# Kernel tuning notes

Measured on AMD Instinct MI355X. Metric: run time of the kernel, lower is better.

Reference implementation:

```python
import jax, jax.numpy as jnp
import numpy as np

N = 100000
E = 1600000
IN_C, HID, OUT_C = 3, 64, 1


def setup_inputs() -> dict:
    key = jax.random.key(0)
    ks = jax.random.split(key, 12)
    x = jax.random.normal(ks[0], (N, IN_C), dtype=jnp.float32)
    edge_index = jax.random.randint(ks[1], (2, E), 0, N, dtype=jnp.int64)

    def glorot(k, shape):
        lim = np.sqrt(6.0 / (shape[0] + shape[1]))
        return jax.random.uniform(k, shape, jnp.float32, -lim, lim)

    return {
        "x": x,
        "edge_index": edge_index,
        "W1": glorot(ks[2], (IN_C, HID)), "b1": jnp.zeros((HID,), jnp.float32),
        "W2": glorot(ks[3], (HID, HID)), "b2": jnp.zeros((HID,), jnp.float32),
        "W3": glorot(ks[4], (HID, HID)), "b3": jnp.zeros((HID,), jnp.float32),
        "Wm1": glorot(ks[5], (HID, HID)), "bm1": jnp.zeros((HID,), jnp.float32),
        "Wm2": glorot(ks[6], (HID, OUT_C)), "bm2": jnp.zeros((OUT_C,), jnp.float32),
    }


def gcn_conv(x, src, dst, W, b):
    """PyG GCNConv: symmetric normalization with self-loops, linear, scatter-add, bias."""
    n = x.shape[0]
    loop = jnp.arange(n, dtype=src.dtype)
    s = jnp.concatenate([src, loop])
    d = jnp.concatenate([dst, loop])
    h = x @ W  # (N, out)
    deg = jax.ops.segment_sum(jnp.ones(s.shape[0], dtype=h.dtype), d, num_segments=n)
    dinv = jnp.where(deg > 0, 1.0 / jnp.sqrt(jnp.where(deg > 0, deg, 1.0)), 0.0)
    norm = dinv[s] * dinv[d]  # (E+N,)
    out = jax.ops.segment_sum(h[s] * norm[:, None], d, num_segments=n)
    return out + b


def reference(x, edge_index, W1, b1, W2, b2, W3, b3, Wm1, bm1, Wm2, bm2):
    src, dst = edge_index[0], edge_index[1]
    # 3 GCN layers with ReLU (dropout inactive in eval mode)
    h = jax.nn.relu(gcn_conv(x, src, dst, W1, b1))
    h = jax.nn.relu(gcn_conv(h, src, dst, W2, b2))
    h = jax.nn.relu(gcn_conv(h, src, dst, W3, b3))
    # MLP head + sigmoid
    h = jax.nn.relu(h @ Wm1 + bm1)
    out = jax.nn.sigmoid(h @ Wm2 + bm2)  # (N, 1)
    return out
```

## Files before the change

kernel.cpp:

```cpp
#include <hip/hip_runtime.h>
#include <hip/hip_fp16.h>
#include <math.h>

#define N_NODES 100000
#define N_EDGES 1600000
#define EP (N_EDGES + N_NODES)
#define HID 64
#define NCHUNK 250
#define CE (N_EDGES / NCHUNK)
#define NBUCK 782
#define CAP 2816
#define NTILE (N_NODES / 16)
#define NPN 4

typedef _Float16 half8_t __attribute__((ext_vector_type(8)));
typedef _Float16 half4_t __attribute__((ext_vector_type(4)));
typedef float f32x4_t __attribute__((ext_vector_type(4)));
typedef unsigned long long u64;


__device__ __forceinline__ float fp8_to_f32_1(unsigned b) {
    unsigned s = b >> 7, e = (b >> 3) & 15, m = b & 7;
    float mag = (e == 0) ? (float)m * 0.001953125f
                         : __uint_as_float(((e + 120u) << 23) | (m << 20));
    return s ? -mag : mag;
}

__device__ __forceinline__ unsigned f32_to_fp8_1(float f) {
    unsigned sb = (__float_as_uint(f) >> 31) << 7;
    float a = fabsf(f);
    if (a > 448.f) a = 448.f;
    if (a < 0.001953125f * 0.5f) return sb;
    if (a < 0.015625f) {
        int q = (int)(a * 512.f + 0.5f);
        if (q > 7) return sb | (1u << 3);
        return sb | (unsigned)q;
    }
    unsigned bits = __float_as_uint(a) + (1u << 19);
    int e = (int)((bits >> 23) & 255) - 127;
    unsigned m = (bits >> 20) & 7;
    int ee = e + 7;
    if (ee > 15) { ee = 15; m = 6; }
    return sb | ((unsigned)ee << 3) | m;
}

__device__ __forceinline__ void addp8(float4& a, unsigned w, bool pred) {
    if (pred) {
#if __has_builtin(__builtin_amdgcn_cvt_pk_f32_fp8)
        auto lo = __builtin_amdgcn_cvt_pk_f32_fp8((int)w, false);
        auto hi = __builtin_amdgcn_cvt_pk_f32_fp8((int)w, true);
        a.x += lo[0]; a.y += lo[1]; a.z += hi[0]; a.w += hi[1];
#else
        a.x += fp8_to_f32_1(w & 255);
        a.y += fp8_to_f32_1((w >> 8) & 255);
        a.z += fp8_to_f32_1((w >> 16) & 255);
        a.w += fp8_to_f32_1(w >> 24);
#endif
    }
}

__device__ __forceinline__ unsigned pack_fp8x4(float a, float b, float c, float d) {
#if __has_builtin(__builtin_amdgcn_cvt_pk_fp8_f32)
    int v = 0;
    v = __builtin_amdgcn_cvt_pk_fp8_f32(a, b, v, false);
    v = __builtin_amdgcn_cvt_pk_fp8_f32(c, d, v, true);
    return (unsigned)v;
#else
    return f32_to_fp8_1(a) | (f32_to_fp8_1(b) << 8) |
           (f32_to_fp8_1(c) << 16) | (f32_to_fp8_1(d) << 24);
#endif
}


__global__ void init_kernel(int* __restrict__ gcur, int* __restrict__ csr) {
    int t = threadIdx.x;
    for (int b = t; b < NBUCK; b += 512) gcur[b] = b * CAP;
    if (t < 64) csr[EP + t] = 0;
}

__global__ __launch_bounds__(1024)
void scatter_kernel(const int* __restrict__ src, const int* __restrict__ dst,
                    int* __restrict__ gcur, unsigned* __restrict__ ebuf) {
    __shared__ int hist[NBUCK];
    __shared__ int cur[NBUCK];
    const int tid = threadIdx.x, c = blockIdx.x;
    for (int b = tid; b < NBUCK; b += 1024) hist[b] = 0;
    __syncthreads();
    const int4* d4p = (const int4*)(dst + c * CE);
    const int4* s4p = (const int4*)(src + c * CE);
    const int t0 = tid, t1 = tid + 1024;
    const bool v1 = t1 < CE / 4;
    int4 d0 = d4p[t0], s0 = s4p[t0];
    int4 d1, s1;
    if (v1) { d1 = d4p[t1]; s1 = s4p[t1]; }
    atomicAdd(&hist[d0.x >> 7], 1);
    atomicAdd(&hist[d0.y >> 7], 1);
    atomicAdd(&hist[d0.z >> 7], 1);
    atomicAdd(&hist[d0.w >> 7], 1);
    if (v1) {
        atomicAdd(&hist[d1.x >> 7], 1);
        atomicAdd(&hist[d1.y >> 7], 1);
        atomicAdd(&hist[d1.z >> 7], 1);
        atomicAdd(&hist[d1.w >> 7], 1);
    }
    __syncthreads();
    for (int b = tid; b < NBUCK; b += 1024)
        cur[b] = hist[b] ? atomicAdd(&gcur[b], hist[b]) : 0;
    __syncthreads();
    {
        int p0 = atomicAdd(&cur[d0.x >> 7], 1);
        ebuf[p0] = ((unsigned)(d0.x & 127) << 17) | (unsigned)s0.x;
        int p1 = atomicAdd(&cur[d0.y >> 7], 1);
        ebuf[p1] = ((unsigned)(d0.y & 127) << 17) | (unsigned)s0.y;
        int p2 = atomicAdd(&cur[d0.z >> 7], 1);
        ebuf[p2] = ((unsigned)(d0.z & 127) << 17) | (unsigned)s0.z;
        int p3 = atomicAdd(&cur[d0.w >> 7], 1);
        ebuf[p3] = ((unsigned)(d0.w & 127) << 17) | (unsigned)s0.w;
    }
    if (v1) {
        int p0 = atomicAdd(&cur[d1.x >> 7], 1);
        ebuf[p0] = ((unsigned)(d1.x & 127) << 17) | (unsigned)s1.x;
        int p1 = atomicAdd(&cur[d1.y >> 7], 1);
        ebuf[p1] = ((unsigned)(d1.y & 127) << 17) | (unsigned)s1.y;
        int p2 = atomicAdd(&cur[d1.z >> 7], 1);
        ebuf[p2] = ((unsigned)(d1.z & 127) << 17) | (unsigned)s1.z;
        int p3 = atomicAdd(&cur[d1.w >> 7], 1);
        ebuf[p3] = ((unsigned)(d1.w & 127) << 17) | (unsigned)s1.w;
    }
}

__global__ __launch_bounds__(256)
void rankfill_kernel(const unsigned* __restrict__ ebuf, const int* __restrict__ gcur,
                     int* __restrict__ rowptr, int* __restrict__ csr,
                     float* __restrict__ dinv,
                     const float* __restrict__ x, float4* __restrict__ xd) {
    __shared__ unsigned stash[CAP];
    __shared__ int out[CAP + 128];
    __shared__ int cnt[128];
    __shared__ int cnt2[128];
    __shared__ int rpl8[128];
    __shared__ int wsum[2];
    __shared__ int sR0;
    const int tid = threadIdx.x, b = blockIdx.x;
    if (tid < 128) { cnt[tid] = 0; cnt2[tid] = 0; }
    if (tid == 0) sR0 = 0;
    __syncthreads();

    int acc = 0;
    for (int i = tid; i < b; i += 256) acc += gcur[i] - i * CAP + 128;
    if (acc) atomicAdd(&sR0, acc);

    const int E0 = b * CAP;
    const int RL = gcur[b] - E0;
    for (int off = tid; off < RL; off += 256) {
        unsigned v = ebuf[E0 + off];
        stash[off] = v;
        atomicAdd(&cnt[(v >> 17) & 0x7F], 1);
    }
    __syncthreads();
    const int R0 = sR0;

    const int lane = tid & 63, w = tid >> 6;
    int xcnt = (tid < 128) ? cnt[tid] : 0;
    int inc = xcnt;
#pragma unroll
    for (int off = 1; off < 64; off <<= 1) {
        int y = __shfl_up(inc, off, 64);
        if (lane >= off) inc += y;
    }
    if (lane == 63 && w < 2) wsum[w] = inc;
    __syncthreads();
    if (tid < 128) {
        int base = (w == 1) ? wsum[0] : 0;
        int rel = tid + base + inc - xcnt;
        rpl8[tid] = rel;
        const int n = b * 128 + tid;
        if (n < N_NODES) {
            rowptr[n] = R0 + rel;
            float di = rsqrtf((float)(xcnt + 1));
            dinv[n] = di;
            out[rel + xcnt] = n;
            xd[n] = make_float4(x[n * 3 + 0] * di, x[n * 3 + 1] * di, x[n * 3 + 2] * di, 0.f);
        }
    }
    if (b == NBUCK - 1 && tid == 0) rowptr[N_NODES] = EP;
    __syncthreads();

    for (int off = tid; off < RL; off += 256) {
        unsigned v = stash[off];
        int key = (v >> 17) & 0x7F;
        int r = atomicAdd(&cnt2[key], 1);
        out[rpl8[key] + r] = (int)(v & 0x1FFFFu);
    }
    __syncthreads();

    const int nreal = min(128, N_NODES - b * 128);
    const int lim = RL + nreal;
    for (int i = tid; i < lim; i += 256) csr[R0 + i] = out[i];
}


__device__ __forceinline__ void bfly_store_lds(float4 acc, const float4 b4, float di,
                                               int g, int p, int l, _Float16* __restrict__ tl) {
    acc.x += __shfl_xor(acc.x, 16, 64);
    acc.y += __shfl_xor(acc.y, 16, 64);
    acc.z += __shfl_xor(acc.z, 16, 64);
    acc.w += __shfl_xor(acc.w, 16, 64);
    acc.x += __shfl_xor(acc.x, 32, 64);
    acc.y += __shfl_xor(acc.y, 32, 64);
    acc.z += __shfl_xor(acc.z, 32, 64);
    acc.w += __shfl_xor(acc.w, 32, 64);
    if (g == 0) {
        half4_t hv;
        hv[0] = (_Float16)fmaxf(fmaf(di, acc.x, b4.x), 0.f);
        hv[1] = (_Float16)fmaxf(fmaf(di, acc.y, b4.y), 0.f);
        hv[2] = (_Float16)fmaxf(fmaf(di, acc.z, b4.z), 0.f);
        hv[3] = (_Float16)fmaxf(fmaf(di, acc.w, b4.w), 0.f);
        *(half4_t*)(tl + l * 72 + p * 4) = hv;
    }
}

__device__ __forceinline__ void gather_phase(const unsigned* __restrict__ gfq,
                                             const int* __restrict__ rowptr,
                                             const int* __restrict__ csr,
                                             const float* __restrict__ dinv,
                                             const float* __restrict__ bias,
                                             int n0, int lane, int wid,
                                             _Float16* __restrict__ tl) {
    const int g = lane >> 4, p = lane & 15;
    const int nw = n0 + wid * NPN;
    int rp = rowptr[nw + min(lane, NPN)];
    const float4 b4 = ((const float4*)bias)[p];
    int begv[NPN], cntv[NPN], idxv[NPN];
    int end_prev = __shfl(rp, 0, 64);
#pragma unroll
    for (int i = 0; i < NPN; ++i) {
        int end = __shfl(rp, i + 1, 64);
        begv[i] = end_prev;
        cntv[i] = end - end_prev;
        end_prev = end;
        idxv[i] = (lane < cntv[i]) ? csr[begv[i] + lane] : 0;
    }
    unsigned u[NPN][4];
#pragma unroll
    for (int i = 0; i < NPN; ++i)
#pragma unroll
        for (int k = 0; k < 4; ++k)
            u[i][k] = gfq[(size_t)__shfl(idxv[i], g + 4 * k, 64) * 16 + p];
#pragma unroll
    for (int i = 0; i < NPN; ++i) {
        const int c = cntv[i];
        float4 acc = make_float4(0.f, 0.f, 0.f, 0.f);
        addp8(acc, u[i][0], g + 0 < c);
        addp8(acc, u[i][1], g + 4 < c);
        addp8(acc, u[i][2], g + 8 < c);
        addp8(acc, u[i][3], g + 12 < c);
        if (c > 16) {
#pragma unroll
            for (int k = 4; k < 8; ++k) {
                int e = g + 4 * k;
                int s = __shfl(idxv[i], e, 64);
                addp8(acc, gfq[(size_t)s * 16 + p], e < c);
            }
            if (c > 32) {
                for (int e = 32 + g; e < c; e += 4) {
                    int s = (e < 64) ? __shfl(idxv[i], e, 64) : csr[begv[i] + e];
                    addp8(acc, gfq[(size_t)s * 16 + p], true);
                }
            }
        }
        bfly_store_lds(acc, b4, dinv[nw + i], g, p, wid * NPN + i, tl);
    }
}

__device__ __forceinline__ void mfma_fp8_store(const float* __restrict__ W,
                                               const float* __restrict__ dinv, int n0,
                                               int lane, int wid, int tid,
                                               _Float16* __restrict__ tile,
                                               _Float16* __restrict__ tile2,
                                               unsigned* __restrict__ gf_out) {
    const int kg = lane >> 4, n = lane & 15;
    half8_t B0, B1;
#pragma unroll
    for (int j = 0; j < 8; ++j) {
        B0[j] = (_Float16)W[(kg * 8 + j) * HID + wid * 16 + n];
        B1[j] = (_Float16)W[(32 + kg * 8 + j) * HID + wid * 16 + n];
    }
    half8_t A0 = *(const half8_t*)(tile + n * 72 + kg * 8);
    half8_t A1 = *(const half8_t*)(tile + n * 72 + 32 + kg * 8);
    f32x4_t c = {0.f, 0.f, 0.f, 0.f};
    c = __builtin_amdgcn_mfma_f32_16x16x32_f16(A0, B0, c, 0, 0, 0);
    c = __builtin_amdgcn_mfma_f32_16x16x32_f16(A1, B1, c, 0, 0, 0);
    const int q = lane >> 4;
#pragma unroll
    for (int r = 0; r < 4; ++r)
        tile2[(q * 4 + r) * 72 + wid * 16 + n] = (_Float16)(c[r] * dinv[n0 + q * 4 + r]);
    __syncthreads();
    const int row = tid >> 4, seg = tid & 15;
    uint2 v = *(const uint2*)(tile2 + row * 72 + seg * 4);
    __half2 h0 = *(__half2*)&v.x, h1 = *(__half2*)&v.y;
    float2 f0 = __half22float2(h0), f1 = __half22float2(h1);
    gf_out[(size_t)(n0 + row) * 16 + seg] = pack_fp8x4(f0.x, f0.y, f1.x, f1.y);
}


__global__ __launch_bounds__(256, 8)
void fused_layer1_kernel(const float4* __restrict__ xd, const int* __restrict__ rowptr,
                         const int* __restrict__ csr, const float* __restrict__ dinv,
                         const float* __restrict__ b1, const float* __restrict__ W1,
                         const float* __restrict__ W2, unsigned* __restrict__ gf_out) {
    __shared__ __align__(16) _Float16 tile[16 * 72];
    __shared__ __align__(16) _Float16 tile2[16 * 72];
    const int tid = threadIdx.x;
    const int lane = tid & 63, wid = tid >> 6;
    const int n0 = blockIdx.x * 16;

    const int j = lane >> 4, p0 = lane & 15;
    const int l = wid * 4 + j;
    const int node = n0 + l;
    const int beg = rowptr[node], end = rowptr[node + 1];
    float a0 = 0.f, a1 = 0.f, a2 = 0.f;
    for (int e = beg + p0; e < end; e += 16) {
        float4 v = xd[csr[e]];
        a0 += v.x; a1 += v.y; a2 += v.z;
    }
#pragma unroll
    for (int off = 1; off < 16; off <<= 1) {
        a0 += __shfl_xor(a0, off, 64);
        a1 += __shfl_xor(a1, off, 64);
        a2 += __shfl_xor(a2, off, 64);
    }
    const float dd = dinv[node];
    const float4 w0 = ((const float4*)W1)[p0];
    const float4 w1 = ((const float4*)(W1 + HID))[p0];
    const float4 w2 = ((const float4*)(W1 + 2 * HID))[p0];
    const float4 bb = ((const float4*)b1)[p0];
    half4_t hv;
    hv[0] = (_Float16)fmaxf(fmaf(dd, a0 * w0.x + a1 * w1.x + a2 * w2.x, bb.x), 0.f);
    hv[1] = (_Float16)fmaxf(fmaf(dd, a0 * w0.y + a1 * w1.y + a2 * w2.y, bb.y), 0.f);
    hv[2] = (_Float16)fmaxf(fmaf(dd, a0 * w0.z + a1 * w1.z + a2 * w2.z, bb.z), 0.f);
    hv[3] = (_Float16)fmaxf(fmaf(dd, a0 * w0.w + a1 * w1.w + a2 * w2.w, bb.w), 0.f);
    *(half4_t*)(tile + l * 72 + p0 * 4) = hv;
    __syncthreads();

    mfma_fp8_store(W2, dinv, n0, lane, wid, tid, tile, tile2, gf_out);
}

__global__ __launch_bounds__(256, 8)
void fused_layer_kernel(const unsigned* __restrict__ gf_in, const int* __restrict__ rowptr,
                        const int* __restrict__ csr, const float* __restrict__ dinv,
                        const float* __restrict__ bias, const float* __restrict__ W,
                        unsigned* __restrict__ gf_out) {
    __shared__ __align__(16) _Float16 tile[16 * 72];
    __shared__ __align__(16) _Float16 tile2[16 * 72];
    const int tid = threadIdx.x;
    const int lane = tid & 63, wid = tid >> 6;
    const int n0 = blockIdx.x * 16;

    gather_phase(gf_in, rowptr, csr, dinv, bias, n0, lane, wid, tile);
    __syncthreads();

    mfma_fp8_store(W, dinv, n0, lane, wid, tid, tile, tile2, gf_out);
}


__global__ __launch_bounds__(256, 8)
void fused_final_kernel(const unsigned* __restrict__ gf_in, const int* __restrict__ rowptr,
                        const int* __restrict__ csr, const float* __restrict__ dinv,
                        const float* __restrict__ b3, const float* __restrict__ Wm1,
                        const float* __restrict__ bm1, const float* __restrict__ Wm2,
                        const float* __restrict__ bm2, float* __restrict__ out) {
    __shared__ __align__(16) _Float16 tile[16 * 72];
    __shared__ float redbuf[4][16];
    const int tid = threadIdx.x;
    const int lane = tid & 63, wid = tid >> 6;
    const int n0 = blockIdx.x * 16;

    gather_phase(gf_in, rowptr, csr, dinv, b3, n0, lane, wid, tile);
    __syncthreads();

    const int kg = lane >> 4, n = lane & 15;
    half8_t B0, B1;
#pragma unroll
    for (int j = 0; j < 8; ++j) {
        B0[j] = (_Float16)Wm1[(kg * 8 + j) * HID + wid * 16 + n];
        B1[j] = (_Float16)Wm1[(32 + kg * 8 + j) * HID + wid * 16 + n];
    }
    half8_t A0 = *(const half8_t*)(tile + n * 72 + kg * 8);
    half8_t A1 = *(const half8_t*)(tile + n * 72 + 32 + kg * 8);
    f32x4_t c = {0.f, 0.f, 0.f, 0.f};
    c = __builtin_amdgcn_mfma_f32_16x16x32_f16(A0, B0, c, 0, 0, 0);
    c = __builtin_amdgcn_mfma_f32_16x16x32_f16(A1, B1, c, 0, 0, 0);

    const float bm1c = bm1[wid * 16 + n];
    const float wm2c = Wm2[wid * 16 + n];
    float part[4];
#pragma unroll
    for (int r = 0; r < 4; ++r) part[r] = fmaxf(c[r] + bm1c, 0.0f) * wm2c;
#pragma unroll
    for (int off = 1; off < 16; off <<= 1)
#pragma unroll
        for (int r = 0; r < 4; ++r) part[r] += __shfl_xor(part[r], off, 64);
    const int q = lane >> 4;
    if (n == 0) {
#pragma unroll
        for (int r = 0; r < 4; ++r) redbuf[wid][q * 4 + r] = part[r];
    }
    __syncthreads();
    if (tid < 16) {
        float s = redbuf[0][tid] + redbuf[1][tid] + redbuf[2][tid] + redbuf[3][tid];
        out[n0 + tid] = 1.0f / (1.0f + expf(-(s + bm2[0])));
    }
}


extern "C" void kernel_launch(void* const* d_in, const int* in_sizes, int n_in,
                              void* d_out, int out_size, void* d_ws, size_t ws_size,
                              hipStream_t stream) {
    const float* x   = (const float*)d_in[0];
    const int*   ei  = (const int*)d_in[1];
    const float* W1  = (const float*)d_in[2];
    const float* b1  = (const float*)d_in[3];
    const float* W2  = (const float*)d_in[4];
    const float* b2  = (const float*)d_in[5];
    const float* W3  = (const float*)d_in[6];
    const float* b3  = (const float*)d_in[7];
    const float* Wm1 = (const float*)d_in[8];
    const float* bm1 = (const float*)d_in[9];
    const float* Wm2 = (const float*)d_in[10];
    const float* bm2 = (const float*)d_in[11];
    float* out = (float*)d_out;

    const int* src = ei;
    const int* dst = ei + N_EDGES;

    char* ws = (char*)d_ws;
    size_t off = 0;
    auto alloc = [&](size_t bytes) { size_t o = off; off = (off + bytes + 255) & ~(size_t)255; return (void*)(ws + o); };
    int*      rowptr = (int*)alloc(4ll * (N_NODES + 1));
    int*      gcur   = (int*)alloc(4ll * NBUCK);
    int*      csr    = (int*)alloc(4ll * (EP + 64));
    float*    dinv   = (float*)alloc(4ll * N_NODES);
    float4*   xd     = (float4*)alloc(16ll * N_NODES);
    unsigned* gfA    = (unsigned*)alloc(4ll * N_NODES * 16);
    unsigned* gfB    = (unsigned*)alloc(4ll * N_NODES * 16);
    unsigned* ebuf   = (unsigned*)alloc(4ll * (size_t)NBUCK * CAP);
    (void)ws_size;

    init_kernel<<<1, 512, 0, stream>>>(gcur, csr);
    scatter_kernel<<<NCHUNK, 1024, 0, stream>>>(src, dst, gcur, ebuf);
    rankfill_kernel<<<NBUCK, 256, 0, stream>>>(ebuf, gcur, rowptr, csr, dinv, x, xd);

    fused_layer1_kernel<<<NTILE, 256, 0, stream>>>(xd, rowptr, csr, dinv, b1, W1, W2, gfB);
    fused_layer_kernel<<<NTILE, 256, 0, stream>>>(gfB, rowptr, csr, dinv, b2, W3, gfA);
    fused_final_kernel<<<NTILE, 256, 0, stream>>>(gfA, rowptr, csr, dinv, b3, Wm1, bm1, Wm2, bm2, out);
}
```

Measured before the change: 193.2 us.

## Split each row's neighbours by source half and gather in two passes

The CSR build now orders each row's neighbours by whether the source node falls in the lower or upper half of the node range, and records a split pointer per row. Layers 2 and 3 each gather in two passes: a new kernel sums the lower-half sources into an fp32 partial buffer, then the fused layer kernel sums the upper-half sources, adds the partial, and continues. The aim is to shrink the gathered feature working set per pass so it fits in cache, and to pair two nodes per iteration for more loads in flight. The cost is two extra kernel launches and writing and rereading a large fp32 partial buffer.

```diff
diff --git a/kernel.cpp b/kernel.cpp
--- a/kernel.cpp
+++ b/kernel.cpp
@@ -12,6 +12,7 @@
 #define CAP 2816
 #define NTILE (N_NODES / 16)
 #define NPN 4
+#define NHALF 50000
 
 typedef _Float16 half8_t __attribute__((ext_vector_type(8)));
 typedef _Float16 half4_t __attribute__((ext_vector_type(4)));
@@ -129,20 +130,20 @@
     }
 }
 
+
 __global__ __launch_bounds__(256)
 void rankfill_kernel(const unsigned* __restrict__ ebuf, const int* __restrict__ gcur,
-                     int* __restrict__ rowptr, int* __restrict__ csr,
-                     float* __restrict__ dinv,
+                     int* __restrict__ rowptr, int* __restrict__ rowsplit,
+                     int* __restrict__ csr, float* __restrict__ dinv,
                      const float* __restrict__ x, float4* __restrict__ xd) {
     __shared__ unsigned stash[CAP];
     __shared__ int out[CAP + 128];
-    __shared__ int cnt[128];
-    __shared__ int cnt2[128];
-    __shared__ int rpl8[128];
+    __shared__ int cntA[128], cntB[128], curA[128], curB[128];
+    __shared__ int relA[128], relB[128];
     __shared__ int wsum[2];
     __shared__ int sR0;
     const int tid = threadIdx.x, b = blockIdx.x;
-    if (tid < 128) { cnt[tid] = 0; cnt2[tid] = 0; }
+    if (tid < 128) { cntA[tid] = 0; cntB[tid] = 0; curA[tid] = 0; curB[tid] = 0; }
     if (tid == 0) sR0 = 0;
     __syncthreads();
 
@@ -155,13 +156,17 @@
     for (int off = tid; off < RL; off += 256) {
         unsigned v = ebuf[E0 + off];
         stash[off] = v;
-        atomicAdd(&cnt[(v >> 17) & 0x7F], 1);
+        int key = (v >> 17) & 0x7F;
+        if ((v & 0x1FFFFu) < (unsigned)NHALF) atomicAdd(&cntA[key], 1);
+        else atomicAdd(&cntB[key], 1);
     }
     __syncthreads();
     const int R0 = sR0;
 
     const int lane = tid & 63, w = tid >> 6;
-    int xcnt = (tid < 128) ? cnt[tid] : 0;
+    int dA = (tid < 128) ? cntA[tid] : 0;
+    int dB = (tid < 128) ? cntB[tid] : 0;
+    int xcnt = dA + dB;
     int inc = xcnt;
 #pragma unroll
     for (int off = 1; off < 64; off <<= 1) {
@@ -173,13 +178,16 @@
     if (tid < 128) {
         int base = (w == 1) ? wsum[0] : 0;
         int rel = tid + base + inc - xcnt;
-        rpl8[tid] = rel;
         const int n = b * 128 + tid;
+        const bool nA = (n < NHALF);
+        relA[tid] = rel;
+        relB[tid] = rel + dA + (nA ? 1 : 0);
         if (n < N_NODES) {
             rowptr[n] = R0 + rel;
+            rowsplit[n] = R0 + rel + dA + (nA ? 1 : 0);
             float di = rsqrtf((float)(xcnt + 1));
             dinv[n] = di;
-            out[rel + xcnt] = n;
+            out[nA ? (rel + dA) : (rel + dA + dB)] = n;
             xd[n] = make_float4(x[n * 3 + 0] * di, x[n * 3 + 1] * di, x[n * 3 + 2] * di, 0.f);
         }
     }
@@ -189,8 +197,9 @@
     for (int off = tid; off < RL; off += 256) {
         unsigned v = stash[off];
         int key = (v >> 17) & 0x7F;
-        int r = atomicAdd(&cnt2[key], 1);
-        out[rpl8[key] + r] = (int)(v & 0x1FFFFu);
+        int s = (int)(v & 0x1FFFFu);
+        if (s < NHALF) { int r = atomicAdd(&curA[key], 1); out[relA[key] + r] = s; }
+        else           { int r = atomicAdd(&curB[key], 1); out[relB[key] + r] = s; }
     }
     __syncthreads();
 
@@ -200,76 +209,150 @@
 }
 
 
-__device__ __forceinline__ void bfly_store_lds(float4 acc, const float4 b4, float di,
-                                               int g, int p, int l, _Float16* __restrict__ tl) {
-    acc.x += __shfl_xor(acc.x, 16, 64);
-    acc.y += __shfl_xor(acc.y, 16, 64);
-    acc.z += __shfl_xor(acc.z, 16, 64);
-    acc.w += __shfl_xor(acc.w, 16, 64);
-    acc.x += __shfl_xor(acc.x, 32, 64);
-    acc.y += __shfl_xor(acc.y, 32, 64);
-    acc.z += __shfl_xor(acc.z, 32, 64);
-    acc.w += __shfl_xor(acc.w, 32, 64);
-    if (g == 0) {
-        half4_t hv;
-        hv[0] = (_Float16)fmaxf(fmaf(di, acc.x, b4.x), 0.f);
-        hv[1] = (_Float16)fmaxf(fmaf(di, acc.y, b4.y), 0.f);
-        hv[2] = (_Float16)fmaxf(fmaf(di, acc.z, b4.z), 0.f);
-        hv[3] = (_Float16)fmaxf(fmaf(di, acc.w, b4.w), 0.f);
-        *(half4_t*)(tl + l * 72 + p * 4) = hv;
-    }
-}
-
-__device__ __forceinline__ void gather_phase(const unsigned* __restrict__ gfq,
-                                             const int* __restrict__ rowptr,
-                                             const int* __restrict__ csr,
-                                             const float* __restrict__ dinv,
-                                             const float* __restrict__ bias,
-                                             int n0, int lane, int wid,
-                                             _Float16* __restrict__ tl) {
+__device__ __forceinline__ void bfly_reduce(float4& a) {
+    a.x += __shfl_xor(a.x, 16, 64);
+    a.y += __shfl_xor(a.y, 16, 64);
+    a.z += __shfl_xor(a.z, 16, 64);
+    a.w += __shfl_xor(a.w, 16, 64);
+    a.x += __shfl_xor(a.x, 32, 64);
+    a.y += __shfl_xor(a.y, 32, 64);
+    a.z += __shfl_xor(a.z, 32, 64);
+    a.w += __shfl_xor(a.w, 32, 64);
+}
+
+#define GATHER_PAIR_BODY(accA, accB, iva, ivb, ca, cb, ba, bb)                              \
+    {                                                                                       \
+        int sa0 = __shfl(iva, g, 64),      sb0 = __shfl(ivb, g, 64);                        \
+        int sa1 = __shfl(iva, g + 4, 64),  sb1 = __shfl(ivb, g + 4, 64);                    \
+        int sa2 = __shfl(iva, g + 8, 64),  sb2 = __shfl(ivb, g + 8, 64);                    \
+        int sa3 = __shfl(iva, g + 12, 64), sb3 = __shfl(ivb, g + 12, 64);                   \
+        unsigned ua0 = gfq[(size_t)sa0 * 16 + p], ub0 = gfq[(size_t)sb0 * 16 + p];          \
+        unsigned ua1 = gfq[(size_t)sa1 * 16 + p], ub1 = gfq[(size_t)sb1 * 16 + p];          \
+        unsigned ua2 = gfq[(size_t)sa2 * 16 + p], ub2 = gfq[(size_t)sb2 * 16 + p];          \
+        unsigned ua3 = gfq[(size_t)sa3 * 16 + p], ub3 = gfq[(size_t)sb3 * 16 + p];          \
+        addp8(accA, ua0, g + 0 < ca);  addp8(accB, ub0, g + 0 < cb);                        \
+        addp8(accA, ua1, g + 4 < ca);  addp8(accB, ub1, g + 4 < cb);                        \
+        addp8(accA, ua2, g + 8 < ca);  addp8(accB, ub2, g + 8 < cb);                        \
+        addp8(accA, ua3, g + 12 < ca); addp8(accB, ub3, g + 12 < cb);                       \
+        if (ca > 16) {                                                                      \
+            _Pragma("unroll")                                                               \
+            for (int k = 4; k < 8; ++k) {                                                   \
+                int e = g + 4 * k;                                                          \
+                int s = __shfl(iva, e, 64);                                                 \
+                addp8(accA, gfq[(size_t)s * 16 + p], e < ca);                               \
+            }                                                                               \
+            if (ca > 32) {                                                                  \
+                for (int e = 32 + g; e < ca; e += 4) {                                      \
+                    int s = (e < 64) ? __shfl(iva, e, 64) : csr[ba + e];                    \
+                    addp8(accA, gfq[(size_t)s * 16 + p], true);                             \
+                }                                                                           \
+            }                                                                               \
+        }                                                                                   \
+        if (cb > 16) {                                                                      \
+            _Pragma("unroll")                                                               \
+            for (int k = 4; k < 8; ++k) {                                                   \
+                int e = g + 4 * k;                                                          \
+                int s = __shfl(ivb, e, 64);                                                 \
+                addp8(accB, gfq[(size_t)s * 16 + p], e < cb);                               \
+            }                                                                               \
+            if (cb > 32) {                                                                  \
+                for (int e = 32 + g; e < cb; e += 4) {                                      \
+                    int s = (e < 64) ? __shfl(ivb, e, 64) : csr[bb + e];                    \
+                    addp8(accB, gfq[(size_t)s * 16 + p], true);                             \
+                }                                                                           \
+            }                                                                               \
+        }                                                                                   \
+    }
+
+
+__global__ __launch_bounds__(256, 8)
+void gpassA_kernel(const unsigned* __restrict__ gfq, const int* __restrict__ rowptr,
+                   const int* __restrict__ rowsplit, const int* __restrict__ csr,
+                   f32x4_t* __restrict__ part) {
+    const int tid = threadIdx.x;
+    const int lane = tid & 63, wid = tid >> 6;
+    const int n0 = blockIdx.x * 16;
     const int g = lane >> 4, p = lane & 15;
     const int nw = n0 + wid * NPN;
-    int rp = rowptr[nw + min(lane, NPN)];
+    int rpv = (lane < NPN) ? rowptr[nw + lane] : 0;
+    int spv = (lane < NPN) ? rowsplit[nw + lane] : 0;
+    int begv[NPN], cntv[NPN], idxv[NPN];
+#pragma unroll
+    for (int i = 0; i < NPN; ++i) {
+        begv[i] = __shfl(rpv, i, 64);
+        cntv[i] = __shfl(spv, i, 64) - begv[i];
+        idxv[i] = (lane < cntv[i]) ? csr[begv[i] + lane] : 0;
+    }
+#pragma unroll
+    for (int ii = 0; ii < NPN; ii += 2) {
+        const int ca = cntv[ii], cb = cntv[ii + 1];
+        const int ba = begv[ii], bb = begv[ii + 1];
+        const int iva = idxv[ii], ivb = idxv[ii + 1];
+        float4 accA = make_float4(0.f, 0.f, 0.f, 0.f);
+        float4 accB = make_float4(0.f, 0.f, 0.f, 0.f);
+        GATHER_PAIR_BODY(accA, accB, iva, ivb, ca, cb, ba, bb)
+        bfly_reduce(accA);
+        bfly_reduce(accB);
+        if (g == 0) {
+            f32x4_t tA; tA[0] = accA.x; tA[1] = accA.y; tA[2] = accA.z; tA[3] = accA.w;
+            __builtin_nontemporal_store(tA, part + (((size_t)(nw + ii)) << 4) + p);
+            f32x4_t tB; tB[0] = accB.x; tB[1] = accB.y; tB[2] = accB.z; tB[3] = accB.w;
+            __builtin_nontemporal_store(tB, part + (((size_t)(nw + ii + 1)) << 4) + p);
+        }
+    }
+}
+
+
+__device__ __forceinline__ void gather_phaseB(const unsigned* __restrict__ gfq,
+                                              const int* __restrict__ rowptr,
+                                              const int* __restrict__ rowsplit,
+                                              const int* __restrict__ csr,
+                                              const float* __restrict__ dinv,
+                                              const float* __restrict__ bias,
+                                              const f32x4_t* __restrict__ part,
+                                              int n0, int lane, int wid,
+                                              _Float16* __restrict__ tl) {
+    const int g = lane >> 4, p = lane & 15;
+    const int nw = n0 + wid * NPN;
+    int rpv = rowptr[nw + min(lane, NPN)];
+    int spv = (lane < NPN) ? rowsplit[nw + lane] : 0;
     const float4 b4 = ((const float4*)bias)[p];
     int begv[NPN], cntv[NPN], idxv[NPN];
-    int end_prev = __shfl(rp, 0, 64);
 #pragma unroll
     for (int i = 0; i < NPN; ++i) {
-        int end = __shfl(rp, i + 1, 64);
-        begv[i] = end_prev;
-        cntv[i] = end - end_prev;
-        end_prev = end;
+        begv[i] = __shfl(spv, i, 64);
+        cntv[i] = __shfl(rpv, i + 1, 64) - begv[i];
         idxv[i] = (lane < cntv[i]) ? csr[begv[i] + lane] : 0;
     }
-    unsigned u[NPN][4];
-#pragma unroll
-    for (int i = 0; i < NPN; ++i)
-#pragma unroll
-        for (int k = 0; k < 4; ++k)
-            u[i][k] = gfq[(size_t)__shfl(idxv[i], g + 4 * k, 64) * 16 + p];
-#pragma unroll
-    for (int i = 0; i < NPN; ++i) {
-        const int c = cntv[i];
-        float4 acc = make_float4(0.f, 0.f, 0.f, 0.f);
-        addp8(acc, u[i][0], g + 0 < c);
-        addp8(acc, u[i][1], g + 4 < c);
-        addp8(acc, u[i][2], g + 8 < c);
-        addp8(acc, u[i][3], g + 12 < c);
-        if (c > 16) {
-#pragma unroll
-            for (int k = 4; k < 8; ++k) {
-                int e = g + 4 * k;
-                int s = __shfl(idxv[i], e, 64);
-                addp8(acc, gfq[(size_t)s * 16 + p], e < c);
-            }
-            if (c > 32) {
-                for (int e = 32 + g; e < c; e += 4) {
-                    int s = (e < 64) ? __shfl(idxv[i], e, 64) : csr[begv[i] + e];
-                    addp8(acc, gfq[(size_t)s * 16 + p], true);
-                }
-            }
+#pragma unroll
+    for (int ii = 0; ii < NPN; ii += 2) {
+        const int la = wid * NPN + ii, lb = la + 1;
+        const int ca = cntv[ii], cb = cntv[ii + 1];
+        const int ba = begv[ii], bb = begv[ii + 1];
+        const int iva = idxv[ii], ivb = idxv[ii + 1];
+        float4 accA = make_float4(0.f, 0.f, 0.f, 0.f);
+        float4 accB = make_float4(0.f, 0.f, 0.f, 0.f);
+        GATHER_PAIR_BODY(accA, accB, iva, ivb, ca, cb, ba, bb)
+        bfly_reduce(accA);
+        bfly_reduce(accB);
+        if (g == 0) {
+            f32x4_t pfA = __builtin_nontemporal_load(part + (((size_t)(n0 + la)) << 4) + p);
+            f32x4_t pfB = __builtin_nontemporal_load(part + (((size_t)(n0 + lb)) << 4) + p);
+            accA.x += pfA[0]; accA.y += pfA[1]; accA.z += pfA[2]; accA.w += pfA[3];
+            accB.x += pfB[0]; accB.y += pfB[1]; accB.z += pfB[2]; accB.w += pfB[3];
+            const float diA = dinv[n0 + la], diB = dinv[n0 + lb];
+            half4_t hvA, hvB;
+            hvA[0] = (_Float16)fmaxf(fmaf(diA, accA.x, b4.x), 0.f);
+            hvA[1] = (_Float16)fmaxf(fmaf(diA, accA.y, b4.y), 0.f);
+            hvA[2] = (_Float16)fmaxf(fmaf(diA, accA.z, b4.z), 0.f);
+            hvA[3] = (_Float16)fmaxf(fmaf(diA, accA.w, b4.w), 0.f);
+            *(half4_t*)(tl + la * 72 + p * 4) = hvA;
+            hvB[0] = (_Float16)fmaxf(fmaf(diB, accB.x, b4.x), 0.f);
+            hvB[1] = (_Float16)fmaxf(fmaf(diB, accB.y, b4.y), 0.f);
+            hvB[2] = (_Float16)fmaxf(fmaf(diB, accB.z, b4.z), 0.f);
+            hvB[3] = (_Float16)fmaxf(fmaf(diB, accB.w, b4.w), 0.f);
+            *(half4_t*)(tl + lb * 72 + p * 4) = hvB;
         }
-        bfly_store_lds(acc, b4, dinv[nw + i], g, p, wid * NPN + i, tl);
     }
 }
 
@@ -346,18 +429,20 @@
     mfma_fp8_store(W2, dinv, n0, lane, wid, tid, tile, tile2, gf_out);
 }
 
+
 __global__ __launch_bounds__(256, 8)
-void fused_layer_kernel(const unsigned* __restrict__ gf_in, const int* __restrict__ rowptr,
-                        const int* __restrict__ csr, const float* __restrict__ dinv,
-                        const float* __restrict__ bias, const float* __restrict__ W,
-                        unsigned* __restrict__ gf_out) {
+void fused_layerB_kernel(const unsigned* __restrict__ gf_in, const int* __restrict__ rowptr,
+                         const int* __restrict__ rowsplit, const int* __restrict__ csr,
+                         const float* __restrict__ dinv, const float* __restrict__ bias,
+                         const f32x4_t* __restrict__ part, const float* __restrict__ W,
+                         unsigned* __restrict__ gf_out) {
     __shared__ __align__(16) _Float16 tile[16 * 72];
     __shared__ __align__(16) _Float16 tile2[16 * 72];
     const int tid = threadIdx.x;
     const int lane = tid & 63, wid = tid >> 6;
     const int n0 = blockIdx.x * 16;
 
-    gather_phase(gf_in, rowptr, csr, dinv, bias, n0, lane, wid, tile);
+    gather_phaseB(gf_in, rowptr, rowsplit, csr, dinv, bias, part, n0, lane, wid, tile);
     __syncthreads();
 
     mfma_fp8_store(W, dinv, n0, lane, wid, tid, tile, tile2, gf_out);
@@ -365,18 +450,19 @@
 
 
 __global__ __launch_bounds__(256, 8)
-void fused_final_kernel(const unsigned* __restrict__ gf_in, const int* __restrict__ rowptr,
-                        const int* __restrict__ csr, const float* __restrict__ dinv,
-                        const float* __restrict__ b3, const float* __restrict__ Wm1,
-                        const float* __restrict__ bm1, const float* __restrict__ Wm2,
-                        const float* __restrict__ bm2, float* __restrict__ out) {
+void fused_finalB_kernel(const unsigned* __restrict__ gf_in, const int* __restrict__ rowptr,
+                         const int* __restrict__ rowsplit, const int* __restrict__ csr,
+                         const float* __restrict__ dinv, const float* __restrict__ b3,
+                         const f32x4_t* __restrict__ part, const float* __restrict__ Wm1,
+                         const float* __restrict__ bm1, const float* __restrict__ Wm2,
+                         const float* __restrict__ bm2, float* __restrict__ out) {
     __shared__ __align__(16) _Float16 tile[16 * 72];
     __shared__ float redbuf[4][16];
     const int tid = threadIdx.x;
     const int lane = tid & 63, wid = tid >> 6;
     const int n0 = blockIdx.x * 16;
 
-    gather_phase(gf_in, rowptr, csr, dinv, b3, n0, lane, wid, tile);
+    gather_phaseB(gf_in, rowptr, rowsplit, csr, dinv, b3, part, n0, lane, wid, tile);
     __syncthreads();
 
     const int kg = lane >> 4, n = lane & 15;
@@ -394,17 +480,17 @@
 
     const float bm1c = bm1[wid * 16 + n];
     const float wm2c = Wm2[wid * 16 + n];
-    float part[4];
-#pragma unroll
-    for (int r = 0; r < 4; ++r) part[r] = fmaxf(c[r] + bm1c, 0.0f) * wm2c;
+    float part4[4];
+#pragma unroll
+    for (int r = 0; r < 4; ++r) part4[r] = fmaxf(c[r] + bm1c, 0.0f) * wm2c;
 #pragma unroll
     for (int off = 1; off < 16; off <<= 1)
 #pragma unroll
-        for (int r = 0; r < 4; ++r) part[r] += __shfl_xor(part[r], off, 64);
+        for (int r = 0; r < 4; ++r) part4[r] += __shfl_xor(part4[r], off, 64);
     const int q = lane >> 4;
     if (n == 0) {
 #pragma unroll
-        for (int r = 0; r < 4; ++r) redbuf[wid][q * 4 + r] = part[r];
+        for (int r = 0; r < 4; ++r) redbuf[wid][q * 4 + r] = part4[r];
     }
     __syncthreads();
     if (tid < 16) {
@@ -437,21 +523,27 @@
     char* ws = (char*)d_ws;
     size_t off = 0;
     auto alloc = [&](size_t bytes) { size_t o = off; off = (off + bytes + 255) & ~(size_t)255; return (void*)(ws + o); };
-    int*      rowptr = (int*)alloc(4ll * (N_NODES + 1));
-    int*      gcur   = (int*)alloc(4ll * NBUCK);
-    int*      csr    = (int*)alloc(4ll * (EP + 64));
-    float*    dinv   = (float*)alloc(4ll * N_NODES);
-    float4*   xd     = (float4*)alloc(16ll * N_NODES);
-    unsigned* gfA    = (unsigned*)alloc(4ll * N_NODES * 16);
-    unsigned* gfB    = (unsigned*)alloc(4ll * N_NODES * 16);
-    unsigned* ebuf   = (unsigned*)alloc(4ll * (size_t)NBUCK * CAP);
+    int*      rowptr   = (int*)alloc(4ll * (N_NODES + 1));
+    int*      rowsplit = (int*)alloc(4ll * N_NODES);
+    int*      gcur     = (int*)alloc(4ll * NBUCK);
+    int*      csr      = (int*)alloc(4ll * (EP + 64));
+    float*    dinv     = (float*)alloc(4ll * N_NODES);
+    float4*   xd       = (float4*)alloc(16ll * N_NODES);
+    unsigned* gfA      = (unsigned*)alloc(4ll * N_NODES * 16);
+    unsigned* gfB      = (unsigned*)alloc(4ll * N_NODES * 16);
+    f32x4_t*  part     = (f32x4_t*)alloc(16ll * N_NODES * 16);
+    unsigned* ebuf     = (unsigned*)alloc(4ll * (size_t)NBUCK * CAP);
     (void)ws_size;
 
     init_kernel<<<1, 512, 0, stream>>>(gcur, csr);
     scatter_kernel<<<NCHUNK, 1024, 0, stream>>>(src, dst, gcur, ebuf);
-    rankfill_kernel<<<NBUCK, 256, 0, stream>>>(ebuf, gcur, rowptr, csr, dinv, x, xd);
+    rankfill_kernel<<<NBUCK, 256, 0, stream>>>(ebuf, gcur, rowptr, rowsplit, csr, dinv, x, xd);
 
     fused_layer1_kernel<<<NTILE, 256, 0, stream>>>(xd, rowptr, csr, dinv, b1, W1, W2, gfB);
-    fused_layer_kernel<<<NTILE, 256, 0, stream>>>(gfB, rowptr, csr, dinv, b2, W3, gfA);
-    fused_final_kernel<<<NTILE, 256, 0, stream>>>(gfA, rowptr, csr, dinv, b3, Wm1, bm1, Wm2, bm2, out);
-}
+
+    gpassA_kernel<<<NTILE, 256, 0, stream>>>(gfB, rowptr, rowsplit, csr, part);
+    fused_layerB_kernel<<<NTILE, 256, 0, stream>>>(gfB, rowptr, rowsplit, csr, dinv, b2, part, W3, gfA);
+
+    gpassA_kernel<<<NTILE, 256, 0, stream>>>(gfA, rowptr, rowsplit, csr, part);
+    fused_finalB_kernel<<<NTILE, 256, 0, stream>>>(gfA, rowptr, rowsplit, csr, dinv, b3, part, Wm1, bm1, Wm2, bm2, out);
+}
```

Result: slower. 219.1 us (+13.4%).
